# Optimization experiments

Measured on AMD Instinct MI355X. Metric: run time of the kernel, lower is better.

The kernel has to match this reference:

```python
import jax, jax.numpy as jnp
import numpy as np

DIM = 2048
NUM_HEADS = 16
HEAD_DIM = DIM // NUM_HEADS  # 128
LC = HEAD_DIM // 2           # 64 complex pairs per head
B, S = 2, 2048
EPS = 1e-6


def setup_inputs() -> dict:
    key = jax.random.key(0)
    ks = jax.random.split(key, 12)
    x = jax.random.normal(ks[0], (B, S, DIM), dtype=jnp.float32)
    # freqs: unit-modulus complex rotations stored as (cos, sin), shape [S,1,LC,2]
    theta = jax.random.uniform(ks[1], (S, 1, LC), dtype=jnp.float32) * (2.0 * np.pi)
    freqs = jnp.stack([jnp.cos(theta), jnp.sin(theta)], axis=-1)
    scale = 0.02
    wq = jax.random.normal(ks[2], (DIM, DIM), dtype=jnp.float32) * scale
    bq = jnp.zeros((DIM,), dtype=jnp.float32)
    wk = jax.random.normal(ks[3], (DIM, DIM), dtype=jnp.float32) * scale
    bk = jnp.zeros((DIM,), dtype=jnp.float32)
    wv = jax.random.normal(ks[4], (DIM, DIM), dtype=jnp.float32) * scale
    bv = jnp.zeros((DIM,), dtype=jnp.float32)
    wo = jax.random.normal(ks[5], (DIM, DIM), dtype=jnp.float32) * scale
    bo = jnp.zeros((DIM,), dtype=jnp.float32)
    gq = jnp.ones((DIM,), dtype=jnp.float32)   # RMSNorm weight for q
    gk = jnp.ones((DIM,), dtype=jnp.float32)   # RMSNorm weight for k
    return {"x": x, "freqs": freqs, "wq": wq, "bq": bq, "wk": wk, "bk": bk,
            "wv": wv, "bv": bv, "wo": wo, "bo": bo, "gq": gq, "gk": gk}


def _rms_norm(x, g):
    xf = x.astype(jnp.float32)
    y = xf * jax.lax.rsqrt(jnp.mean(xf * xf, axis=-1, keepdims=True) + EPS)
    return y.astype(x.dtype) * g


def _rope_apply(x, freqs):
    # x: [B,S,D] -> complex pairs [B,S,H,LC,2]; freqs: [S,1,LC,2] (cos,sin)
    b, s, _ = x.shape
    xp = x.astype(jnp.float32).reshape(b, s, NUM_HEADS, LC, 2)
    xr, xi = xp[..., 0], xp[..., 1]
    cr = freqs[None, :, :, :, 0]  # [1,S,1,LC]
    ci = freqs[None, :, :, :, 1]
    out_r = xr * cr - xi * ci
    out_i = xr * ci + xi * cr
    out = jnp.stack([out_r, out_i], axis=-1).reshape(b, s, DIM)
    return out.astype(x.dtype)


def _attention(q, k, v):
    # q,k,v: [B,S,D] -> multihead SDPA -> [B,S,D]
    b, s, _ = q.shape
    qh = q.reshape(b, s, NUM_HEADS, HEAD_DIM).transpose(0, 2, 1, 3)
    kh = k.reshape(b, s, NUM_HEADS, HEAD_DIM).transpose(0, 2, 1, 3)
    vh = v.reshape(b, s, NUM_HEADS, HEAD_DIM).transpose(0, 2, 1, 3)
    scale = 1.0 / np.sqrt(HEAD_DIM).astype(np.float32)
    scores = jnp.einsum('bhqd,bhkd->bhqk', qh, kh) * scale
    probs = jax.nn.softmax(scores, axis=-1)
    out = jnp.einsum('bhqk,bhkd->bhqd', probs, vh)
    return out.transpose(0, 2, 1, 3).reshape(b, s, DIM)


def reference(x, freqs, wq, bq, wk, bk, wv, bv, wo, bo, gq, gk):
    q = _rms_norm(x @ wq.T + bq, gq)
    k = _rms_norm(x @ wk.T + bk, gk)
    v = x @ wv.T + bv
    q = _rope_apply(q, freqs)
    k = _rope_apply(k, freqs)
    attn = _attention(q, k, v)
    return attn @ wo.T + bo
```

## Files before the change

kernel.cpp:

```cpp
#include <hip/hip_runtime.h>
#include <cstdint>

typedef __bf16 bf16;
typedef __bf16 bf16x8 __attribute__((ext_vector_type(8)));
typedef __bf16 bf16x4 __attribute__((ext_vector_type(4)));
typedef float f32x4 __attribute__((ext_vector_type(4)));

#define DIMN 2048
#define SEQ  2048
#define NH   16
#define HD   128

__device__ __forceinline__ void gld_lds16(const bf16* g, bf16* l) {
    __builtin_amdgcn_global_load_lds(
        (const __attribute__((address_space(1))) void*)g,
        (__attribute__((address_space(3))) void*)l,
        16, 0, 0);
}

__global__ __launch_bounds__(256) void cast_all(
    const float* __restrict__ x,
    const float* __restrict__ wq, const float* __restrict__ wk,
    const float* __restrict__ wv, const float* __restrict__ wo,
    bf16* __restrict__ xb,
    bf16* __restrict__ wqb, bf16* __restrict__ wkb,
    bf16* __restrict__ wvb, bf16* __restrict__ wob)
{
    int id = blockIdx.x;
    const float* src; bf16* dst; int i;
    if (id < 8192) { src = x; dst = xb; i = id * 256 + threadIdx.x; }
    else {
        id -= 8192;
        int w = id >> 12; id &= 4095;
        src = (w == 0) ? wq : (w == 1) ? wk : (w == 2) ? wv : wo;
        dst = (w == 0) ? wqb : (w == 1) ? wkb : (w == 2) ? wvb : wob;
        i = id * 256 + threadIdx.x;
    }
    float4 v = ((const float4*)src)[i];
    bf16x4 o;
    o[0] = (bf16)v.x; o[1] = (bf16)v.y; o[2] = (bf16)v.z; o[3] = (bf16)v.w;
    ((bf16x4*)dst)[i] = o;
}

template<int OUT_F32>
__global__ __launch_bounds__(256) void gemm_bt(
    const bf16* __restrict__ A,
    const bf16* __restrict__ Bw0, const bf16* __restrict__ Bw1, const bf16* __restrict__ Bw2,
    const float* __restrict__ bias0, const float* __restrict__ bias1, const float* __restrict__ bias2,
    void* __restrict__ C0, void* __restrict__ C1, void* __restrict__ C2)
{
    const int K = DIMN, N = DIMN;
    const bf16* Bw = Bw0; const float* bias = bias0; void* Cout = C0;
    if (blockIdx.z == 1) { Bw = Bw1; bias = bias1; Cout = C1; }
    if (blockIdx.z == 2) { Bw = Bw2; bias = bias2; Cout = C2; }

    __shared__ __attribute__((aligned(16))) bf16 As[128 * 64];
    __shared__ __attribute__((aligned(16))) bf16 Bs[128 * 64];

    const int t    = threadIdx.x;
    const int lane = t & 63, wave = t >> 6;
    const int l15  = lane & 15, quad = lane >> 4;
    const int wm   = (wave >> 1) * 64, wn = (wave & 1) * 64;
    const long bm  = (long)blockIdx.y * 128;
    const long bn  = (long)blockIdx.x * 128;

    const bf16* agp[4]; const bf16* bgp[4]; bf16* asd[4]; bf16* bsd[4];
#pragma unroll
    for (int it = 0; it < 4; it++) {
        int fs  = it * 256 + t;
        int row = fs >> 3;
        int gs  = (fs & 7) ^ (row & 7);
        agp[it] = A  + (bm + row) * (long)K + gs * 8;
        bgp[it] = Bw + (bn + row) * (long)K + gs * 8;
        asd[it] = As + fs * 8;
        bsd[it] = Bs + fs * 8;
    }
    const int swl = l15 & 7;

    f32x4 acc[4][4] = {};

    for (int k0 = 0; k0 < K; k0 += 64) {
#pragma unroll
        for (int it = 0; it < 4; it++) {
            gld_lds16(agp[it] + k0, asd[it]);
            gld_lds16(bgp[it] + k0, bsd[it]);
        }
        __syncthreads();

#pragma unroll
        for (int ks2 = 0; ks2 < 2; ks2++) {
            const int sw = ((ks2 * 4 + quad) ^ swl) * 8;
            bf16x8 af[4], bfr[4];
#pragma unroll
            for (int i = 0; i < 4; i++)
                af[i] = *(const bf16x8*)(As + (wm + i * 16 + l15) * 64 + sw);
#pragma unroll
            for (int j = 0; j < 4; j++)
                bfr[j] = *(const bf16x8*)(Bs + (wn + j * 16 + l15) * 64 + sw);
#pragma unroll
            for (int i = 0; i < 4; i++)
#pragma unroll
                for (int j = 0; j < 4; j++)
                    acc[i][j] = __builtin_amdgcn_mfma_f32_16x16x32_bf16(af[i], bfr[j], acc[i][j], 0, 0, 0);
        }
        __syncthreads();
    }

#pragma unroll
    for (int j = 0; j < 4; j++) {
        const long col = bn + wn + j * 16 + l15;
        const float bv = bias[col];
#pragma unroll
        for (int i = 0; i < 4; i++) {
            const long row0 = bm + wm + i * 16 + quad * 4;
#pragma unroll
            for (int r = 0; r < 4; r++) {
                float v = acc[i][j][r] + bv;
                if (OUT_F32) ((float*)Cout)[(row0 + r) * N + col] = v;
                else         ((bf16*)Cout)[(row0 + r) * N + col] = (bf16)v;
            }
        }
    }
}

__global__ __launch_bounds__(256) void norm_prep(
    bf16* __restrict__ q, bf16* __restrict__ k,
    const float* __restrict__ gq, const float* __restrict__ gk,
    const float* __restrict__ freqs,
    const bf16* __restrict__ vin, bf16* __restrict__ vt)
{
    const int id = blockIdx.x;
    const int t = threadIdx.x;
    if (id < 8192) {
        const int qk  = id >> 12;
        const int row = id & 4095;
        bf16* ptr = qk ? k : q;
        const float* g = qk ? gk : gq;
        const float osc = qk ? 1.0f : 0.08838834764831845f;
        const int s = row & (SEQ - 1);
        const int lane = t & 63, wave = t >> 6;

        bf16* base = ptr + (long)row * DIMN + t * 8;
        bf16x8 raw = *(const bf16x8*)base;
        float v[8]; float ss = 0.f;
#pragma unroll
        for (int j = 0; j < 8; j++) { v[j] = (float)raw[j]; ss += v[j] * v[j]; }
#pragma unroll
        for (int off = 32; off; off >>= 1) ss += __shfl_xor(ss, off, 64);
        __shared__ float red[4];
        if (lane == 0) red[wave] = ss;
        __syncthreads();
        float tot = red[0] + red[1] + red[2] + red[3];
        float rn = rsqrtf(tot * (1.0f / DIMN) + 1e-6f);

        const int e0 = t * 8;
        bf16x8 o;
#pragma unroll
        for (int pp = 0; pp < 4; pp++) {
            int e = e0 + pp * 2;
            float xr = v[pp * 2]     * rn * g[e];
            float xi = v[pp * 2 + 1] * rn * g[e + 1];
            int lc = (e >> 1) & 63;
            float cr = freqs[s * 128 + lc * 2];
            float ci = freqs[s * 128 + lc * 2 + 1];
            o[pp * 2]     = (bf16)((xr * cr - xi * ci) * osc);
            o[pp * 2 + 1] = (bf16)((xr * ci + xi * cr) * osc);
        }
        *(bf16x8*)base = o;
    } else {
        const int tid = id - 8192;
        const int b = tid >> 10, rem = tid & 1023;
        const int st = rem & 31, ct = rem >> 5;
        __shared__ float tile[64][65];
        const int tx = t & 63, ty = t >> 6;
#pragma unroll
        for (int ii = 0; ii < 16; ii++) {
            int r = ii * 4 + ty;
            tile[r][tx] = (float)vin[((long)(b * SEQ + st * 64 + r)) * DIMN + ct * 64 + tx];
        }
        __syncthreads();
#pragma unroll
        for (int ii = 0; ii < 16; ii++) {
            int c = ii * 4 + ty;
            vt[((long)(b * DIMN + ct * 64 + c)) * SEQ + st * 64 + tx] = (bf16)tile[tx][c];
        }
    }
}

__global__ __launch_bounds__(512, 2) void attention(
    const bf16* __restrict__ Q, const bf16* __restrict__ Kb,
    const bf16* __restrict__ Vt, bf16* __restrict__ O)
{
    __shared__ __attribute__((aligned(16))) bf16 Ksh[2][64 * 128];
    __shared__ __attribute__((aligned(16))) bf16 Vsh[2][128 * 64];
    __shared__ __attribute__((aligned(16))) bf16 Psh[8][32 * 72];
    __shared__ float Lsh[8][32];

    const int t = threadIdx.x;
    const int lane = t & 63, w = t >> 6;
    const int l15 = lane & 15, quad = lane >> 4;
    const int bh = blockIdx.x, b = bh >> 4, h = bh & 15;
    const int qt = blockIdx.y;
    const long qrow0 = (long)b * SEQ + qt * 256 + w * 32;
    const bf16* qbase = Q  + qrow0 * DIMN + h * HD;
    const bf16* kbase = Kb + (long)b * SEQ * DIMN + h * HD;
    const bf16* vbase = Vt + (long)bh * HD * SEQ;

    bf16x8 qf[2][4];
#pragma unroll
    for (int im = 0; im < 2; im++)
#pragma unroll
        for (int kd = 0; kd < 4; kd++)
            qf[im][kd] = *(const bf16x8*)(qbase + (long)(im * 16 + l15) * DIMN + kd * 32 + quad * 8);

    long koff[2], voff[2];
#pragma unroll
    for (int it = 0; it < 2; it++) {
        int fs = it * 512 + t;
        int kr = fs >> 4, kp = fs & 15;
        koff[it] = (long)kr * DIMN + (kp ^ (kr & 15)) * 8;
        int dr = fs >> 3, vp = fs & 7;
        voff[it] = (long)dr * SEQ + (vp ^ (dr & 7)) * 8;
    }

    f32x4 o_acc[2][8] = {};
    float Lt[2] = {0.f, 0.f};

#pragma unroll
    for (int it = 0; it < 2; it++) {
        gld_lds16(kbase + koff[it], &Ksh[0][(it * 512 + t) * 8]);
        gld_lds16(vbase + voff[it], &Vsh[0][(it * 512 + t) * 8]);
    }
    __syncthreads();

    for (int kt = 0; kt < 32; kt++) {
        const int cur = kt & 1;
        if (kt < 31) {
            const bf16* kg = kbase + (long)((kt + 1) * 64) * DIMN;
            const bf16* vg = vbase + (kt + 1) * 64;
#pragma unroll
            for (int it = 0; it < 2; it++) {
                gld_lds16(kg + koff[it], &Ksh[cur ^ 1][(it * 512 + t) * 8]);
                gld_lds16(vg + voff[it], &Vsh[cur ^ 1][(it * 512 + t) * 8]);
            }
        }
        const bf16* K0 = Ksh[cur];
        const bf16* V0 = Vsh[cur];

        f32x4 st[4][2] = {};
#pragma unroll
        for (int jk = 0; jk < 4; jk++)
#pragma unroll
            for (int kd = 0; kd < 4; kd++) {
                bf16x8 kf = *(const bf16x8*)(K0 + (jk * 16 + l15) * 128 + (((kd * 4 + quad) ^ l15) & 15) * 8);
                st[jk][0] = __builtin_amdgcn_mfma_f32_16x16x32_bf16(kf, qf[0][kd], st[jk][0], 0, 0, 0);
                st[jk][1] = __builtin_amdgcn_mfma_f32_16x16x32_bf16(kf, qf[1][kd], st[jk][1], 0, 0, 0);
            }

#pragma unroll
        for (int im = 0; im < 2; im++) {
            float part = 0.f;
#pragma unroll
            for (int jk = 0; jk < 4; jk++) {
                bf16x4 pk;
#pragma unroll
                for (int r = 0; r < 4; r++) {
                    float e = __expf(st[jk][im][r]);
                    part += e;
                    pk[r] = (bf16)e;
                }
                *(bf16x4*)(Psh[w] + (im * 16 + l15) * 72 + jk * 16 + quad * 4) = pk;
            }
            Lt[im] += part;
        }

#pragma unroll
        for (int kd2 = 0; kd2 < 2; kd2++) {
            bf16x8 pa[2];
            pa[0] = *(const bf16x8*)(Psh[w] + (l15)      * 72 + kd2 * 32 + quad * 8);
            pa[1] = *(const bf16x8*)(Psh[w] + (16 + l15) * 72 + kd2 * 32 + quad * 8);
#pragma unroll
            for (int dj = 0; dj < 8; dj++) {
                bf16x8 vfr = *(const bf16x8*)(V0 + (dj * 16 + l15) * 64 + (((kd2 * 4 + quad) ^ l15) & 7) * 8);
                o_acc[0][dj] = __builtin_amdgcn_mfma_f32_16x16x32_bf16(pa[0], vfr, o_acc[0][dj], 0, 0, 0);
                o_acc[1][dj] = __builtin_amdgcn_mfma_f32_16x16x32_bf16(pa[1], vfr, o_acc[1][dj], 0, 0, 0);
            }
        }
        __syncthreads();
    }

#pragma unroll
    for (int im = 0; im < 2; im++) {
        Lt[im] += __shfl_xor(Lt[im], 16, 64);
        Lt[im] += __shfl_xor(Lt[im], 32, 64);
    }
    if (quad == 0) { Lsh[w][l15] = Lt[0]; Lsh[w][16 + l15] = Lt[1]; }
    __syncthreads();

#pragma unroll
    for (int im = 0; im < 2; im++)
#pragma unroll
        for (int r = 0; r < 4; r++) {
            float inv = 1.0f / Lsh[w][im * 16 + quad * 4 + r];
            long orow = qrow0 + im * 16 + quad * 4 + r;
#pragma unroll
            for (int dj = 0; dj < 8; dj++)
                O[orow * DIMN + h * HD + dj * 16 + l15] = (bf16)(o_acc[im][dj][r] * inv);
        }
}

extern "C" void kernel_launch(void* const* d_in, const int* in_sizes, int n_in,
                              void* d_out, int out_size, void* d_ws, size_t ws_size,
                              hipStream_t stream) {
    const float* x     = (const float*)d_in[0];
    const float* freqs = (const float*)d_in[1];
    const float* wq    = (const float*)d_in[2];
    const float* bq    = (const float*)d_in[3];
    const float* wk    = (const float*)d_in[4];
    const float* bk    = (const float*)d_in[5];
    const float* wv    = (const float*)d_in[6];
    const float* bv    = (const float*)d_in[7];
    const float* wo    = (const float*)d_in[8];
    const float* bo    = (const float*)d_in[9];
    const float* gq    = (const float*)d_in[10];
    const float* gk    = (const float*)d_in[11];
    float* out = (float*)d_out;

    const size_t MAT  = (size_t)4096 * 2048 * 2;
    const size_t WMAT = (size_t)2048 * 2048 * 2;
    char* p = (char*)d_ws;
    bf16* xb  = (bf16*)p; p += MAT;
    bf16* wqb = (bf16*)p; p += WMAT;
    bf16* wkb = (bf16*)p; p += WMAT;
    bf16* wvb = (bf16*)p; p += WMAT;
    bf16* wob = (bf16*)p; p += WMAT;
    bf16* qb  = (bf16*)p; p += MAT;
    bf16* kb  = (bf16*)p; p += MAT;
    bf16* vb  = (bf16*)p; p += MAT;
    bf16* vt  = (bf16*)p; p += MAT;
    bf16* attn = qb;

    cast_all<<<24576, 256, 0, stream>>>(x, wq, wk, wv, wo, xb, wqb, wkb, wvb, wob);

    gemm_bt<0><<<dim3(16, 32, 3), 256, 0, stream>>>(xb, wqb, wkb, wvb,
                                                    bq, bk, bv, qb, kb, vb);
    norm_prep<<<10240, 256, 0, stream>>>(qb, kb, gq, gk, freqs, vb, vt);
    attention<<<dim3(32, 8), 512, 0, stream>>>(qb, kb, vt, attn);
    gemm_bt<1><<<dim3(16, 32, 1), 256, 0, stream>>>(attn, wob, wob, wob,
                                                    bo, bo, bo, out, out, out);
}
```

Baseline: 392.3 us.

## Fuse V transpose into GEMM epilogue and split QKV projection launches

The V projection GEMM now writes its output already transposed (Vt layout) through a new epilogue mode. This removes the separate transpose branch of the norm kernel and the intermediate V buffer. The single fused QKV launch becomes three separate GEMM launches, and the norm kernel keeps only the RMSNorm+RoPE path. In the attention loop, the barrier moves to the top of each iteration and the barrier before the final row-sum read is dropped. The risks are strided 8-byte stores in the transposed epilogue and reduced per-launch parallelism from splitting the QKV GEMM.

```diff
diff --git a/kernel.cpp b/kernel.cpp
--- a/kernel.cpp
+++ b/kernel.cpp
@@ -42,18 +42,12 @@
     ((bf16x4*)dst)[i] = o;
 }
 
-template<int OUT_F32>
+template<int EPI>
 __global__ __launch_bounds__(256) void gemm_bt(
-    const bf16* __restrict__ A,
-    const bf16* __restrict__ Bw0, const bf16* __restrict__ Bw1, const bf16* __restrict__ Bw2,
-    const float* __restrict__ bias0, const float* __restrict__ bias1, const float* __restrict__ bias2,
-    void* __restrict__ C0, void* __restrict__ C1, void* __restrict__ C2)
+    const bf16* __restrict__ A, const bf16* __restrict__ Bw,
+    const float* __restrict__ bias, void* __restrict__ Cout)
 {
     const int K = DIMN, N = DIMN;
-    const bf16* Bw = Bw0; const float* bias = bias0; void* Cout = C0;
-    if (blockIdx.z == 1) { Bw = Bw1; bias = bias1; Cout = C1; }
-    if (blockIdx.z == 2) { Bw = Bw2; bias = bias2; Cout = C2; }
-
     __shared__ __attribute__((aligned(16))) bf16 As[128 * 64];
     __shared__ __attribute__((aligned(16))) bf16 Bs[128 * 64];
 
@@ -113,78 +107,66 @@
 #pragma unroll
         for (int i = 0; i < 4; i++) {
             const long row0 = bm + wm + i * 16 + quad * 4;
-#pragma unroll
-            for (int r = 0; r < 4; r++) {
-                float v = acc[i][j][r] + bv;
-                if (OUT_F32) ((float*)Cout)[(row0 + r) * N + col] = v;
-                else         ((bf16*)Cout)[(row0 + r) * N + col] = (bf16)v;
-            }
-        }
-    }
-}
-
-__global__ __launch_bounds__(256) void norm_prep(
+            if (EPI == 2) {
+                const long b = row0 >> 11, s0 = row0 & 2047;
+                bf16x4 pk;
+#pragma unroll
+                for (int r = 0; r < 4; r++) pk[r] = (bf16)(acc[i][j][r] + bv);
+                *(bf16x4*)((bf16*)Cout + (b * DIMN + col) * (long)SEQ + s0) = pk;
+            } else {
+#pragma unroll
+                for (int r = 0; r < 4; r++) {
+                    float v = acc[i][j][r] + bv;
+                    if (EPI == 1) ((float*)Cout)[(row0 + r) * N + col] = v;
+                    else          ((bf16*)Cout)[(row0 + r) * N + col] = (bf16)v;
+                }
+            }
+        }
+    }
+}
+
+__global__ __launch_bounds__(256) void rmsnorm_rope(
     bf16* __restrict__ q, bf16* __restrict__ k,
     const float* __restrict__ gq, const float* __restrict__ gk,
-    const float* __restrict__ freqs,
-    const bf16* __restrict__ vin, bf16* __restrict__ vt)
+    const float* __restrict__ freqs)
 {
     const int id = blockIdx.x;
+    const int qk  = id >> 12;
+    const int row = id & 4095;
+    bf16* ptr = qk ? k : q;
+    const float* g = qk ? gk : gq;
+    const float osc = qk ? 1.0f : 0.08838834764831845f;
+    const int s = row & (SEQ - 1);
     const int t = threadIdx.x;
-    if (id < 8192) {
-        const int qk  = id >> 12;
-        const int row = id & 4095;
-        bf16* ptr = qk ? k : q;
-        const float* g = qk ? gk : gq;
-        const float osc = qk ? 1.0f : 0.08838834764831845f;
-        const int s = row & (SEQ - 1);
-        const int lane = t & 63, wave = t >> 6;
-
-        bf16* base = ptr + (long)row * DIMN + t * 8;
-        bf16x8 raw = *(const bf16x8*)base;
-        float v[8]; float ss = 0.f;
-#pragma unroll
-        for (int j = 0; j < 8; j++) { v[j] = (float)raw[j]; ss += v[j] * v[j]; }
-#pragma unroll
-        for (int off = 32; off; off >>= 1) ss += __shfl_xor(ss, off, 64);
-        __shared__ float red[4];
-        if (lane == 0) red[wave] = ss;
-        __syncthreads();
-        float tot = red[0] + red[1] + red[2] + red[3];
-        float rn = rsqrtf(tot * (1.0f / DIMN) + 1e-6f);
-
-        const int e0 = t * 8;
-        bf16x8 o;
-#pragma unroll
-        for (int pp = 0; pp < 4; pp++) {
-            int e = e0 + pp * 2;
-            float xr = v[pp * 2]     * rn * g[e];
-            float xi = v[pp * 2 + 1] * rn * g[e + 1];
-            int lc = (e >> 1) & 63;
-            float cr = freqs[s * 128 + lc * 2];
-            float ci = freqs[s * 128 + lc * 2 + 1];
-            o[pp * 2]     = (bf16)((xr * cr - xi * ci) * osc);
-            o[pp * 2 + 1] = (bf16)((xr * ci + xi * cr) * osc);
-        }
-        *(bf16x8*)base = o;
-    } else {
-        const int tid = id - 8192;
-        const int b = tid >> 10, rem = tid & 1023;
-        const int st = rem & 31, ct = rem >> 5;
-        __shared__ float tile[64][65];
-        const int tx = t & 63, ty = t >> 6;
-#pragma unroll
-        for (int ii = 0; ii < 16; ii++) {
-            int r = ii * 4 + ty;
-            tile[r][tx] = (float)vin[((long)(b * SEQ + st * 64 + r)) * DIMN + ct * 64 + tx];
-        }
-        __syncthreads();
-#pragma unroll
-        for (int ii = 0; ii < 16; ii++) {
-            int c = ii * 4 + ty;
-            vt[((long)(b * DIMN + ct * 64 + c)) * SEQ + st * 64 + tx] = (bf16)tile[tx][c];
-        }
-    }
+    const int lane = t & 63, wave = t >> 6;
+
+    bf16* base = ptr + (long)row * DIMN + t * 8;
+    bf16x8 raw = *(const bf16x8*)base;
+    float v[8]; float ss = 0.f;
+#pragma unroll
+    for (int j = 0; j < 8; j++) { v[j] = (float)raw[j]; ss += v[j] * v[j]; }
+#pragma unroll
+    for (int off = 32; off; off >>= 1) ss += __shfl_xor(ss, off, 64);
+    __shared__ float red[4];
+    if (lane == 0) red[wave] = ss;
+    __syncthreads();
+    float tot = red[0] + red[1] + red[2] + red[3];
+    float rn = rsqrtf(tot * (1.0f / DIMN) + 1e-6f);
+
+    const int e0 = t * 8;
+    bf16x8 o;
+#pragma unroll
+    for (int pp = 0; pp < 4; pp++) {
+        int e = e0 + pp * 2;
+        float xr = v[pp * 2]     * rn * g[e];
+        float xi = v[pp * 2 + 1] * rn * g[e + 1];
+        int lc = (e >> 1) & 63;
+        float cr = freqs[s * 128 + lc * 2];
+        float ci = freqs[s * 128 + lc * 2 + 1];
+        o[pp * 2]     = (bf16)((xr * cr - xi * ci) * osc);
+        o[pp * 2 + 1] = (bf16)((xr * ci + xi * cr) * osc);
+    }
+    *(bf16x8*)base = o;
 }
 
 __global__ __launch_bounds__(512, 2) void attention(
@@ -231,10 +213,10 @@
         gld_lds16(kbase + koff[it], &Ksh[0][(it * 512 + t) * 8]);
         gld_lds16(vbase + voff[it], &Vsh[0][(it * 512 + t) * 8]);
     }
-    __syncthreads();
 
     for (int kt = 0; kt < 32; kt++) {
         const int cur = kt & 1;
+        __syncthreads();
         if (kt < 31) {
             const bf16* kg = kbase + (long)((kt + 1) * 64) * DIMN;
             const bf16* vg = vbase + (kt + 1) * 64;
@@ -286,7 +268,6 @@
                 o_acc[1][dj] = __builtin_amdgcn_mfma_f32_16x16x32_bf16(pa[1], vfr, o_acc[1][dj], 0, 0, 0);
             }
         }
-        __syncthreads();
     }
 
 #pragma unroll
@@ -295,7 +276,6 @@
         Lt[im] += __shfl_xor(Lt[im], 32, 64);
     }
     if (quad == 0) { Lsh[w][l15] = Lt[0]; Lsh[w][16 + l15] = Lt[1]; }
-    __syncthreads();
 
 #pragma unroll
     for (int im = 0; im < 2; im++)
@@ -336,16 +316,16 @@
     bf16* wob = (bf16*)p; p += WMAT;
     bf16* qb  = (bf16*)p; p += MAT;
     bf16* kb  = (bf16*)p; p += MAT;
-    bf16* vb  = (bf16*)p; p += MAT;
     bf16* vt  = (bf16*)p; p += MAT;
     bf16* attn = qb;
 
     cast_all<<<24576, 256, 0, stream>>>(x, wq, wk, wv, wo, xb, wqb, wkb, wvb, wob);
 
-    gemm_bt<0><<<dim3(16, 32, 3), 256, 0, stream>>>(xb, wqb, wkb, wvb,
-                                                    bq, bk, bv, qb, kb, vb);
-    norm_prep<<<10240, 256, 0, stream>>>(qb, kb, gq, gk, freqs, vb, vt);
+    gemm_bt<0><<<dim3(16, 32), 256, 0, stream>>>(xb, wqb, bq, qb);
+    gemm_bt<0><<<dim3(16, 32), 256, 0, stream>>>(xb, wkb, bk, kb);
+    gemm_bt<2><<<dim3(16, 32), 256, 0, stream>>>(xb, wvb, bv, vt);
+
+    rmsnorm_rope<<<8192, 256, 0, stream>>>(qb, kb, gq, gk, freqs);
     attention<<<dim3(32, 8), 512, 0, stream>>>(qb, kb, vt, attn);
-    gemm_bt<1><<<dim3(16, 32, 1), 256, 0, stream>>>(attn, wob, wob, wob,
-                                                    bo, bo, bo, out, out, out);
-}
+    gemm_bt<1><<<dim3(16, 32), 256, 0, stream>>>(attn, wob, bo, out);
+}
```

New measurement: 404.4 us. +3.1%, slower.
